# Kernel optimization log

Measured on AMD Instinct MI355X. Metric: run time of the kernel, lower is better.

## Reference

```python
import jax, jax.numpy as jnp
import numpy as np

NA, NC = 5, 20          # num_anchors, num_classes
EPS, SLOPE = 1e-5, 0.1  # BatchNorm eps, LeakyReLU slope


def _conv(x, w, pad):
    return jax.lax.conv_general_dilated(
        x, w, (1, 1), [(pad, pad), (pad, pad)],
        dimension_numbers=("NCHW", "OIHW", "NCHW"))


def _cbl(x, w, g, b, m, v, pad):
    # Conv2dBatchLeaky: conv (no bias) + eval-mode BN + LeakyReLU(0.1)
    x = _conv(x, w, pad)
    scale = (g * jax.lax.rsqrt(v + EPS))[None, :, None, None]
    shift = (b - m * g * jax.lax.rsqrt(v + EPS))[None, :, None, None]
    x = x * scale + shift
    return jnp.where(x > 0, x, SLOPE * x)


def _reorg(x, s=2):
    # faithful lightnet Reorg: out channels = s*s*C, spatial halved
    B, C, H, W = x.shape
    x = x.reshape(B, C, H // s, s, W // s, s)
    x = x.transpose(0, 1, 2, 4, 3, 5)                 # B,C,H/s,W/s,s,s
    x = x.reshape(B, C, (H // s) * (W // s), s * s)
    x = x.transpose(0, 1, 3, 2)                        # B,C,s*s,HW/s^2
    x = x.reshape(B, C, s * s, H // s, W // s)
    x = x.transpose(0, 2, 1, 3, 4)                     # B,s*s,C,H/s,W/s
    return x.reshape(B, s * s * C, H // s, W // s)


def setup_inputs() -> dict:
    key = jax.random.key(0)
    ks = jax.random.split(key, 16)
    B = 16
    return {
        "feat0": jax.random.normal(ks[0], (B, 1024, 19, 19), jnp.float32),
        "feat1": jax.random.normal(ks[1], (B, 512, 38, 38), jnp.float32),
        "w1": jax.random.normal(ks[2], (64, 512, 1, 1), jnp.float32) * 0.05,
        "g1": jax.random.uniform(ks[3], (64,), jnp.float32, 0.5, 1.5),
        "b1": jax.random.normal(ks[4], (64,), jnp.float32) * 0.05,
        "m1": jax.random.normal(ks[5], (64,), jnp.float32) * 0.05,
        "v1": jax.random.uniform(ks[6], (64,), jnp.float32, 0.5, 1.5),
        "w2": jax.random.normal(ks[7], (1024, 1280, 3, 3), jnp.float32) * 0.01,
        "g2": jax.random.uniform(ks[8], (1024,), jnp.float32, 0.5, 1.5),
        "b2": jax.random.normal(ks[9], (1024,), jnp.float32) * 0.05,
        "m2": jax.random.normal(ks[10], (1024,), jnp.float32) * 0.05,
        "v2": jax.random.uniform(ks[11], (1024,), jnp.float32, 0.5, 1.5),
        "wd": jax.random.normal(ks[12], (30, 1024, 1, 1), jnp.float32) * 0.02,
        "bd": jax.random.normal(ks[13], (30,), jnp.float32) * 0.02,
    }


def reference(feat0, feat1, w1, g1, b1, m1, v1, w2, g2, b2, m2, v2, wd, bd):
    stage6_reorg = _reorg(_cbl(feat1, w1, g1, b1, m1, v1, pad=0))   # B,256,19,19
    pre = _cbl(jnp.concatenate([stage6_reorg, feat0], axis=1),
               w2, g2, b2, m2, v2, pad=1)                            # B,1024,19,19
    B, C, H, W = pre.shape
    # one-hot reweighting mask: channel c belongs to class (c mod NC)
    rew = (jnp.mod(jnp.arange(C, dtype=jnp.float32), NC)[None, :]
           == jnp.arange(NC, dtype=jnp.float32)[:, None]).astype(pre.dtype)  # NC,C
    tiled = pre[:, None] * rew[None, :, :, None, None]               # B,NC,C,H,W
    pred = _conv(tiled.reshape(B * NC, C, H, W), wd, pad=0) \
        + bd[None, :, None, None]                                    # B*NC,30,H,W
    gp = pred.reshape(B, NC, NA, 6, H, W).transpose(0, 2, 1, 3, 4, 5)  # B,NA,NC,6,H,W
    cls = gp[:, :, :, 5]                                             # B,NA,NC,H,W
    ids = jnp.argmax(cls, axis=2)                                    # B,NA,H,W
    g05 = jnp.take_along_axis(gp[:, :, :, :5],
                              ids[:, :, None, None], axis=2)[:, :, 0]  # B,NA,5,H,W
    final = jnp.concatenate([g05, cls], axis=2)                      # B,NA,25,H,W
    return final.reshape(B, NA * (5 + NC), H, W)
```

## Files before the change

kernel.cpp:

```cpp
#include <hip/hip_runtime.h>
#include <hip/hip_bf16.h>

#define EPSV 1e-5f
#define SLOPEV 0.1f
#define AS1 __attribute__((address_space(1)))
#define AS3 __attribute__((address_space(3)))

typedef __attribute__((ext_vector_type(8))) _Float16 h8;
typedef __attribute__((ext_vector_type(4))) float f32x4;
typedef unsigned int uint32;
typedef unsigned short ushort_t;

#define PLANE       ((size_t)18063360)
#define WSPLIT_OFF  ((size_t)36126720)
#define PRE_OFF     ((size_t)124968960)

#define APREC  28224
#define ABUF   56448
#define BOFF   112896
#define BBUF   24576
#define SMEMSZ 162048

__device__ __forceinline__ void split2_pack(const float* f, uint32* ph, uint32* pm) {
#pragma unroll
  for (int i = 0; i < 4; ++i) {
    float a = f[2 * i], b = f[2 * i + 1];
    _Float16 ha = (_Float16)a, hb = (_Float16)b;
    float ra = (a - (float)ha) * 2048.f;
    float rb = (b - (float)hb) * 2048.f;
    _Float16 ma = (_Float16)ra, mb = (_Float16)rb;
    ph[i] = (uint32)__builtin_bit_cast(ushort_t, ha) | ((uint32)__builtin_bit_cast(ushort_t, hb) << 16);
    pm[i] = (uint32)__builtin_bit_cast(ushort_t, ma) | ((uint32)__builtin_bit_cast(ushort_t, mb) << 16);
  }
}

__global__ __launch_bounds__(256) void k_conv1(
    const float* __restrict__ feat1, const float* __restrict__ w1,
    const float* __restrict__ g1, const float* __restrict__ b1,
    const float* __restrict__ m1, const float* __restrict__ v1,
    char* __restrict__ nbase)
{
  __shared__ __attribute__((aligned(16))) float S[16384];
  const int bid = blockIdx.x;
  const int bx = bid % 12, cqq = (bid / 12) & 1, b = bid / 24;
  const int t = threadIdx.x;

#pragma unroll
  for (int i = 0; i < 16; ++i) {
    int f4 = t + i * 256;
    int j = f4 >> 7, c4 = (f4 & 127) * 4;
    *(float4*)&S[j * 512 + c4] = *(const float4*)&w1[(cqq * 32 + j) * 512 + c4];
  }
  __syncthreads();

  const int cq16 = t >> 7;
  const int cq = cqq * 2 + cq16;
  const int p = bx * 128 + (t & 127);
  const int pp = p < 1444 ? p : 1443;
  const float* xp = feat1 + (size_t)(b * 512) * 1444 + pp;
  float acc[16];
#pragma unroll
  for (int j = 0; j < 16; ++j) acc[j] = 0.f;
#pragma unroll 2
  for (int c4 = 0; c4 < 512; c4 += 4) {
    float x0 = xp[(size_t)(c4 + 0) * 1444];
    float x1 = xp[(size_t)(c4 + 1) * 1444];
    float x2 = xp[(size_t)(c4 + 2) * 1444];
    float x3 = xp[(size_t)(c4 + 3) * 1444];
#pragma unroll
    for (int j = 0; j < 16; ++j) {
      float4 w = *(const float4*)&S[(cq16 * 16 + j) * 512 + c4];
      acc[j] = fmaf(x0, w.x, acc[j]);
      acc[j] = fmaf(x1, w.y, acc[j]);
      acc[j] = fmaf(x2, w.z, acc[j]);
      acc[j] = fmaf(x3, w.w, acc[j]);
    }
  }
  if (p >= 1444) return;
#pragma unroll
  for (int j = 0; j < 16; ++j) {
    int co = cq * 16 + j;
    float sc = g1[co] / sqrtf(v1[co] + EPSV);
    float sh = b1[co] - m1[co] * sc;
    float v = fmaf(acc[j], sc, sh);
    acc[j] = v > 0.f ? v : SLOPEV * v;
  }
  int y = p / 38, x = p - (p / 38) * 38;
  int q = ((y & 1) << 1) | (x & 1);
  int s = (1 + (y >> 1)) * 21 + 1 + (x >> 1);
  const int sw = (s >> 1) & 3;
  size_t rowb = ((size_t)(b * 441 + s)) * 2560;
  int grp = (q * 64 + cq * 16) >> 5;
  char* d0 = nbase + rowb + grp * 64;
#pragma unroll
  for (int u = 0; u < 2; ++u) {
    int q4 = ((cq & 1) << 1) | u;
    uint32 H[4], M[4];
    split2_pack(&acc[u * 8], H, M);
    int off = (q4 ^ sw) << 4;
    *(uint4*)(d0 + off)         = make_uint4(H[0], H[1], H[2], H[3]);
    *(uint4*)(d0 + PLANE + off) = make_uint4(M[0], M[1], M[2], M[3]);
  }
}

__global__ __launch_bounds__(256) void k_prep(
    const float* __restrict__ feat0, const float* __restrict__ w2,
    char* __restrict__ nbase, char* __restrict__ wsp)
{
  __shared__ __attribute__((aligned(16))) float S[8192];
  const int bid = blockIdx.x;
  const int t = threadIdx.x;

  if (bid < 1600) {
    int gid = bid * 256 + t;
    int c16 = gid % 160;
    int r = gid / 160;
    int bp = r % 80;
    int pi = r / 80;
    int s;
    if (bp < 21) s = bp;
    else if (bp < 42) s = 399 + bp;
    else if (bp < 61) s = (bp - 41) * 21;
    else s = (bp - 60) * 21 + 20;
    int plane = pi >> 4, img = pi & 15;
    *(uint4*)(nbase + (size_t)plane * PLANE + ((size_t)(img * 441 + s)) * 2560 + c16 * 16)
        = make_uint4(0u, 0u, 0u, 0u);

  } else if (bid < 4160) {
    const int blk = bid - 1600;
    const int cc = blk >> 6, nt = (blk >> 2) & 15, nj = blk & 3;
    const float* src = w2 + ((size_t)(nt * 64 + nj * 16) * 1280 + cc * 32) * 9;
#pragma unroll
    for (int i = 0; i < 18; ++i) {
      int idx = t + i * 256;
      int col = idx / 288, d = idx - col * 288;
      S[col * 289 + d] = src[(size_t)col * 11520 + d];
    }
    __syncthreads();
#pragma unroll
    for (int it = 0; it < 3; ++it) {
      int u = t + it * 256;
      if (u < 576) {
        int tap = u / 64, kq = (u >> 4) & 3, ln = u & 15;
        float f[8];
#pragma unroll
        for (int c8 = 0; c8 < 8; ++c8) f[c8] = S[ln * 289 + (kq * 8 + c8) * 9 + tap] * 32.f;
        uint32 H[4], M[4];
        split2_pack(f, H, M);
        size_t ob = ((size_t)(cc * 16 + nt) * 9 + tap) * 8192 + nj * 1024
                  + (kq * 16 + ln) * 16;
        *(uint4*)(wsp + ob)        = make_uint4(H[0], H[1], H[2], H[3]);
        *(uint4*)(wsp + ob + 4096) = make_uint4(M[0], M[1], M[2], M[3]);
      }
    }

  } else {
    const int bid4 = bid - 4160;
    const int px = bid4 % 6, cy = (bid4 / 6) % 16, b = bid4 / 96;
    const int p0 = px * 64, c0 = 256 + cy * 64;
#pragma unroll
    for (int j = 0; j < 16; ++j) {
      int c_l = (t >> 6) + j * 4;
      int p_l = t & 63;
      float v = 0.f;
      int pos = p0 + p_l;
      if (pos < 361)
        v = feat0[((size_t)(b * 1024 + (c0 - 256) + c_l)) * 361 + pos];
      S[c_l * 65 + p_l] = v;
    }
    __syncthreads();
#pragma unroll
    for (int jj = 0; jj < 2; ++jj) {
      int p_l = (t >> 3) + jj * 32;
      int cgrp = t & 7;
      int pos = p0 + p_l;
      if (pos < 361) {
        int y = pos / 19, x = pos - (pos / 19) * 19;
        int s = (y + 1) * 21 + x + 1;
        float f[8];
#pragma unroll
        for (int u = 0; u < 8; ++u) f[u] = S[(cgrp * 8 + u) * 65 + p_l];
        uint32 H[4], M[4];
        split2_pack(f, H, M);
        int ch8 = c0 + cgrp * 8;
        int grp = ch8 >> 5, q4 = (ch8 >> 3) & 3;
        size_t byteo = ((size_t)(b * 441 + s)) * 2560 + grp * 64
                     + ((q4 ^ ((s >> 1) & 3)) << 4);
        *(uint4*)(nbase + byteo)         = make_uint4(H[0], H[1], H[2], H[3]);
        *(uint4*)(nbase + PLANE + byteo) = make_uint4(M[0], M[1], M[2], M[3]);
      }
    }
  }
}

__global__ __launch_bounds__(512, 2) void k_conv2(
    const char* __restrict__ nbase, const char* __restrict__ wsp,
    const float* __restrict__ g2, const float* __restrict__ b2,
    const float* __restrict__ m2, const float* __restrict__ v2,
    float* __restrict__ pre)
{
  __shared__ __attribute__((aligned(16))) unsigned char smem[SMEMSZ];

  const int bid = blockIdx.x;
  const int img = (bid & 7) * 2 + ((bid >> 3) & 1);
  const int ntile = (bid >> 4) & 15;
  const int co0 = ntile * 64;

  const int tid = threadIdx.x;
  const int wv = tid >> 6;
  const int lane = tid & 63;
  const int ln = lane & 15;
  const int q = lane >> 4;

  int arow[3];
#pragma unroll
  for (int mi = 0; mi < 3; ++mi) {
    int p = wv * 48 + mi * 16 + ln;
    p = p > 360 ? 360 : p;
    arow[mi] = (p / 19) * 21 + (p - (p / 19) * 19);
  }

  f32x4 acc0[3][4], acc1[3][4];
#pragma unroll
  for (int mi = 0; mi < 3; ++mi)
#pragma unroll
    for (int nj = 0; nj < 4; ++nj) { acc0[mi][nj] = (f32x4)0.f; acc1[mi][nj] = (f32x4)0.f; }

  const size_t imgbase = (size_t)(img * 441) * 2560;
  const size_t wnt = (size_t)ntile * 9 * 8192;

#pragma unroll
  for (int i = 0; i < 7; ++i) {
    int idx = tid + i * 512;
    if (idx < 3528) {
      int pr = idx / 1764;
      int r  = idx - pr * 1764;
      const char* src = nbase + (size_t)pr * PLANE + imgbase
                      + (size_t)(r >> 2) * 2560 + ((r & 3) << 4);
      __builtin_amdgcn_global_load_lds((const AS1 uint32*)src,
          (AS3 uint32*)(smem + idx * 16), 16, 0, 0);
    }
  }
  {
    const char* bs = wsp + wnt;
#pragma unroll
    for (int i = 0; i < 3; ++i) {
      int idx = tid + i * 512;
      __builtin_amdgcn_global_load_lds((const AS1 uint32*)(bs + idx * 16),
          (AS3 uint32*)(smem + BOFF + idx * 16), 16, 0, 0);
    }
  }
  __syncthreads();

#pragma unroll 1
  for (int cc = 0; cc < 1280; cc += 32) {
    const int cur = (cc >> 5) & 1;
    const unsigned char* aCur = smem + cur * ABUF;
    char* aNext = (char*)smem + (cur ^ 1) * ABUF;
    const int ccn = cc + 32;
    const bool pn = ccn < 1280;

#pragma unroll
    for (int p = 0; p < 3; ++p) {
      const int P = (cc >> 5) * 3 + p;
      if (P + 1 < 120) {
        const int nc = (P + 1) / 3, ntb = ((P + 1) - nc * 3) * 3;
        const char* bs = wsp + ((size_t)nc * 144 + (size_t)ntb) * 8192 + wnt;
        char* bd = (char*)smem + BOFF + ((P + 1) & 1) * BBUF;
#pragma unroll
        for (int i = 0; i < 3; ++i) {
          int idx = tid + i * 512;
          __builtin_amdgcn_global_load_lds((const AS1 uint32*)(bs + idx * 16),
              (AS3 uint32*)(bd + idx * 16), 16, 0, 0);
        }
      }
      if (pn) {
#pragma unroll
        for (int i = 0; i < 3; ++i) {
          int idx = p * 1176 + i * 512 + tid;
          if (idx < (p + 1) * 1176) {
            int pr = idx / 1764;
            int r  = idx - pr * 1764;
            const char* src = nbase + (size_t)pr * PLANE + imgbase
                            + (size_t)(r >> 2) * 2560 + (ccn << 1) + ((r & 3) << 4);
            __builtin_amdgcn_global_load_lds((const AS1 uint32*)src,
                (AS3 uint32*)(aNext + idx * 16), 16, 0, 0);
          }
        }
      }

      const unsigned char* bufR = smem + BOFF + (P & 1) * BBUF;
      __builtin_amdgcn_s_setprio(1);
#pragma unroll
      for (int t3 = 0; t3 < 3; ++t3) {
        const int trow = p * 21 + t3;
        h8 A0[3], A1[3];
#pragma unroll
        for (int mi = 0; mi < 3; ++mi) {
          int srow = arow[mi] + trow;
          int aoff = srow * 64 + ((q ^ ((srow >> 1) & 3)) << 4);
          A0[mi] = *(const h8*)(aCur + aoff);
          A1[mi] = *(const h8*)(aCur + APREC + aoff);
        }
#pragma unroll
        for (int nj = 0; nj < 4; ++nj) {
          const unsigned char* bp0 = bufR + t3 * 8192 + nj * 1024 + lane * 16;
          h8 B0 = *(const h8*)(bp0);
          h8 B1 = *(const h8*)(bp0 + 4096);
#pragma unroll
          for (int mi = 0; mi < 3; ++mi) {
            acc0[mi][nj] = __builtin_amdgcn_mfma_f32_16x16x32_f16(A0[mi], B0, acc0[mi][nj], 0, 0, 0);
            acc1[mi][nj] = __builtin_amdgcn_mfma_f32_16x16x32_f16(A0[mi], B1, acc1[mi][nj], 0, 0, 0);
            acc1[mi][nj] = __builtin_amdgcn_mfma_f32_16x16x32_f16(A1[mi], B0, acc1[mi][nj], 0, 0, 0);
          }
        }
      }
      __builtin_amdgcn_s_setprio(0);
      __syncthreads();
    }
  }

#pragma unroll
  for (int nj = 0; nj < 4; ++nj) {
    int co = co0 + nj * 16 + ln;
    float sc = g2[co] / sqrtf(v2[co] + EPSV) * 0.03125f;
    float sh = b2[co] - m2[co] * (sc * 32.f);
    float* op = pre + ((size_t)(img * 1024 + co)) * 361;
#pragma unroll
    for (int mi = 0; mi < 3; ++mi) {
#pragma unroll
      for (int r = 0; r < 4; ++r) {
        int p = wv * 48 + mi * 16 + q * 4 + r;
        if (p < 361) {
          float t = fmaf(acc1[mi][nj][r], 4.8828125e-4f, acc0[mi][nj][r]);
          float v = fmaf(t, sc, sh);
          v = v > 0.f ? v : SLOPEV * v;
          op[p] = v;
        }
      }
    }
  }
}

__global__ __launch_bounds__(384) void k_pred(
    const float* __restrict__ pre, const float* __restrict__ wd,
    const float* __restrict__ bd, float* __restrict__ pred)
{
  __shared__ float W[30 * 52];
  const int k = blockIdx.x;
  const int b = blockIdx.y;
  const int t = threadIdx.x;
  const int nj = (1023 - k) / 20 + 1;

  for (int u = t; u < 30 * 52; u += 384) {
    int o = u / 52, j = u - o * 52;
    W[u] = (j < nj) ? wd[o * 1024 + k + 20 * j] : 0.f;
  }
  __syncthreads();
  if (t >= 361) return;

  const float* xb = pre + (size_t)b * 1024 * 361 + t;
  float acc[30];
#pragma unroll
  for (int o = 0; o < 30; ++o) acc[o] = 0.f;
  for (int j = 0; j < nj; ++j) {
    float x = xb[(size_t)(k + 20 * j) * 361];
#pragma unroll
    for (int o = 0; o < 30; ++o) acc[o] = fmaf(W[o * 52 + j], x, acc[o]);
  }
  float* ob = pred + ((size_t)(b * 20 + k) * 30) * 361 + t;
#pragma unroll
  for (int o = 0; o < 30; ++o) ob[(size_t)o * 361] = acc[o] + bd[o];
}

__global__ __launch_bounds__(64) void k_sel(
    const float* __restrict__ pred, float* __restrict__ out)
{
  const int ph = blockIdx.x, a = blockIdx.y, b = blockIdx.z;
  const int p = ph * 64 + threadIdx.x;
  const bool act = p < 361;
  const int pp = act ? p : 360;
  const float* pb = pred + (size_t)b * 20 * 30 * 361 + pp;

  float best = -3.4e38f; int bidx = 0;
  float cls[20];
#pragma unroll
  for (int kk = 0; kk < 20; ++kk) {
    float s = pb[(size_t)(kk * 30 + a * 6 + 5) * 361];
    cls[kk] = s;
    if (s > best) { best = s; bidx = kk; }
  }
  if (!act) return;
#pragma unroll
  for (int kk = 0; kk < 20; ++kk)
    out[((size_t)(b * 125 + a * 25 + 5 + kk)) * 361 + p] = cls[kk];
#pragma unroll
  for (int j = 0; j < 5; ++j)
    out[((size_t)(b * 125 + a * 25 + j)) * 361 + p]
        = pb[(size_t)(bidx * 30 + a * 6 + j) * 361];
}

extern "C" void kernel_launch(void* const* d_in, const int* in_sizes, int n_in,
                              void* d_out, int out_size, void* d_ws, size_t ws_size,
                              hipStream_t stream)
{
  const float* feat0 = (const float*)d_in[0];
  const float* feat1 = (const float*)d_in[1];
  const float* w1    = (const float*)d_in[2];
  const float* g1    = (const float*)d_in[3];
  const float* b1    = (const float*)d_in[4];
  const float* m1    = (const float*)d_in[5];
  const float* v1    = (const float*)d_in[6];
  const float* w2    = (const float*)d_in[7];
  const float* g2    = (const float*)d_in[8];
  const float* b2    = (const float*)d_in[9];
  const float* m2    = (const float*)d_in[10];
  const float* v2    = (const float*)d_in[11];
  const float* wd    = (const float*)d_in[12];
  const float* bd    = (const float*)d_in[13];
  float* out = (float*)d_out;

  char*  nbase = (char*)d_ws;
  char*  wsp   = (char*)d_ws + WSPLIT_OFF;
  float* pre   = (float*)((char*)d_ws + PRE_OFF);
  float* pred  = (float*)((char*)d_ws + WSPLIT_OFF);

  k_conv1<<<dim3(384), 256, 0, stream>>>(feat1, w1, g1, b1, m1, v1, nbase);
  k_prep<<<dim3(5696), 256, 0, stream>>>(feat0, w2, nbase, wsp);
  k_conv2<<<dim3(256), 512, 0, stream>>>(nbase, wsp, g2, b2, m2, v2, pre);
  k_pred<<<dim3(20, 16), 384, 0, stream>>>(pre, wd, bd, pred);
  k_sel<<<dim3(6, 5, 16), 64, 0, stream>>>(pred, out);
}
```

Measured before the change: 432.8 us.

## Fold conv1 into prep kernel with two pixels per thread

The separate 1x1 conv1 kernel becomes the first 192 blocks of the k_prep launch, which removes one kernel launch and lets conv1 run alongside the zero-fill and weight-split blocks. Each thread now computes two pixel positions (128 apart), so the shared-memory weight reads are reused across twice the work and half as many blocks are needed. The cost is more registers per thread (32 accumulators) and a larger static shared allocation (64KB) for all k_prep blocks, which can cut occupancy of the other prep branches.

```diff
diff --git a/kernel.cpp b/kernel.cpp
--- a/kernel.cpp
+++ b/kernel.cpp
@@ -34,57 +34,8 @@
   }
 }
 
-__global__ __launch_bounds__(256) void k_conv1(
-    const float* __restrict__ feat1, const float* __restrict__ w1,
-    const float* __restrict__ g1, const float* __restrict__ b1,
-    const float* __restrict__ m1, const float* __restrict__ v1,
-    char* __restrict__ nbase)
-{
-  __shared__ __attribute__((aligned(16))) float S[16384];
-  const int bid = blockIdx.x;
-  const int bx = bid % 12, cqq = (bid / 12) & 1, b = bid / 24;
-  const int t = threadIdx.x;
-
-#pragma unroll
-  for (int i = 0; i < 16; ++i) {
-    int f4 = t + i * 256;
-    int j = f4 >> 7, c4 = (f4 & 127) * 4;
-    *(float4*)&S[j * 512 + c4] = *(const float4*)&w1[(cqq * 32 + j) * 512 + c4];
-  }
-  __syncthreads();
-
-  const int cq16 = t >> 7;
-  const int cq = cqq * 2 + cq16;
-  const int p = bx * 128 + (t & 127);
-  const int pp = p < 1444 ? p : 1443;
-  const float* xp = feat1 + (size_t)(b * 512) * 1444 + pp;
-  float acc[16];
-#pragma unroll
-  for (int j = 0; j < 16; ++j) acc[j] = 0.f;
-#pragma unroll 2
-  for (int c4 = 0; c4 < 512; c4 += 4) {
-    float x0 = xp[(size_t)(c4 + 0) * 1444];
-    float x1 = xp[(size_t)(c4 + 1) * 1444];
-    float x2 = xp[(size_t)(c4 + 2) * 1444];
-    float x3 = xp[(size_t)(c4 + 3) * 1444];
-#pragma unroll
-    for (int j = 0; j < 16; ++j) {
-      float4 w = *(const float4*)&S[(cq16 * 16 + j) * 512 + c4];
-      acc[j] = fmaf(x0, w.x, acc[j]);
-      acc[j] = fmaf(x1, w.y, acc[j]);
-      acc[j] = fmaf(x2, w.z, acc[j]);
-      acc[j] = fmaf(x3, w.w, acc[j]);
-    }
-  }
-  if (p >= 1444) return;
-#pragma unroll
-  for (int j = 0; j < 16; ++j) {
-    int co = cq * 16 + j;
-    float sc = g1[co] / sqrtf(v1[co] + EPSV);
-    float sh = b1[co] - m1[co] * sc;
-    float v = fmaf(acc[j], sc, sh);
-    acc[j] = v > 0.f ? v : SLOPEV * v;
-  }
+__device__ __forceinline__ void conv1_store(char* __restrict__ nbase, const float* acc,
+                                            int b, int p, int cq) {
   int y = p / 38, x = p - (p / 38) * 38;
   int q = ((y & 1) << 1) | (x & 1);
   int s = (1 + (y >> 1)) * 21 + 1 + (x >> 1);
@@ -104,15 +55,74 @@
 }
 
 __global__ __launch_bounds__(256) void k_prep(
+    const float* __restrict__ feat1, const float* __restrict__ w1,
+    const float* __restrict__ g1, const float* __restrict__ b1,
+    const float* __restrict__ m1, const float* __restrict__ v1,
     const float* __restrict__ feat0, const float* __restrict__ w2,
     char* __restrict__ nbase, char* __restrict__ wsp)
 {
-  __shared__ __attribute__((aligned(16))) float S[8192];
+  __shared__ __attribute__((aligned(16))) float S[16384];
   const int bid = blockIdx.x;
   const int t = threadIdx.x;
 
-  if (bid < 1600) {
-    int gid = bid * 256 + t;
+  if (bid < 192) {
+    const int bx = bid % 6, cqq = (bid / 6) & 1, b = bid / 12;
+#pragma unroll
+    for (int i = 0; i < 16; ++i) {
+      int f4 = t + i * 256;
+      int j = f4 >> 7, c4 = (f4 & 127) * 4;
+      *(float4*)&S[j * 512 + c4] = *(const float4*)&w1[(cqq * 32 + j) * 512 + c4];
+    }
+    __syncthreads();
+    const int t2 = t & 127;
+    const int cq16 = t >> 7;
+    const int cq = cqq * 2 + cq16;
+    const int pA = bx * 256 + t2;
+    const int pB = pA + 128;
+    const int ppB = pB < 1444 ? pB : 1443;
+    const float* xpA = feat1 + (size_t)(b * 512) * 1444 + pA;
+    const float* xpB = feat1 + (size_t)(b * 512) * 1444 + ppB;
+    float accA[16], accB[16];
+#pragma unroll
+    for (int j = 0; j < 16; ++j) { accA[j] = 0.f; accB[j] = 0.f; }
+#pragma unroll 2
+    for (int c4 = 0; c4 < 512; c4 += 4) {
+      float a0 = xpA[(size_t)(c4 + 0) * 1444];
+      float a1 = xpA[(size_t)(c4 + 1) * 1444];
+      float a2 = xpA[(size_t)(c4 + 2) * 1444];
+      float a3 = xpA[(size_t)(c4 + 3) * 1444];
+      float e0 = xpB[(size_t)(c4 + 0) * 1444];
+      float e1 = xpB[(size_t)(c4 + 1) * 1444];
+      float e2 = xpB[(size_t)(c4 + 2) * 1444];
+      float e3 = xpB[(size_t)(c4 + 3) * 1444];
+#pragma unroll
+      for (int j = 0; j < 16; ++j) {
+        float4 w = *(const float4*)&S[(cq16 * 16 + j) * 512 + c4];
+        accA[j] = fmaf(a0, w.x, accA[j]);
+        accA[j] = fmaf(a1, w.y, accA[j]);
+        accA[j] = fmaf(a2, w.z, accA[j]);
+        accA[j] = fmaf(a3, w.w, accA[j]);
+        accB[j] = fmaf(e0, w.x, accB[j]);
+        accB[j] = fmaf(e1, w.y, accB[j]);
+        accB[j] = fmaf(e2, w.z, accB[j]);
+        accB[j] = fmaf(e3, w.w, accB[j]);
+      }
+    }
+#pragma unroll
+    for (int j = 0; j < 16; ++j) {
+      int co = cq * 16 + j;
+      float sc = g1[co] / sqrtf(v1[co] + EPSV);
+      float sh = b1[co] - m1[co] * sc;
+      float va = fmaf(accA[j], sc, sh);
+      accA[j] = va > 0.f ? va : SLOPEV * va;
+      float vb = fmaf(accB[j], sc, sh);
+      accB[j] = vb > 0.f ? vb : SLOPEV * vb;
+    }
+    conv1_store(nbase, accA, b, pA, cq);
+    if (pB < 1444) conv1_store(nbase, accB, b, pB, cq);
+
+  } else if (bid < 1792) {
+    int gid = (bid - 192) * 256 + t;
     int c16 = gid % 160;
     int r = gid / 160;
     int bp = r % 80;
@@ -126,8 +136,8 @@
     *(uint4*)(nbase + (size_t)plane * PLANE + ((size_t)(img * 441 + s)) * 2560 + c16 * 16)
         = make_uint4(0u, 0u, 0u, 0u);
 
-  } else if (bid < 4160) {
-    const int blk = bid - 1600;
+  } else if (bid < 4352) {
+    const int blk = bid - 1792;
     const int cc = blk >> 6, nt = (blk >> 2) & 15, nj = blk & 3;
     const float* src = w2 + ((size_t)(nt * 64 + nj * 16) * 1280 + cc * 32) * 9;
 #pragma unroll
@@ -155,7 +165,7 @@
     }
 
   } else {
-    const int bid4 = bid - 4160;
+    const int bid4 = bid - 4352;
     const int px = bid4 % 6, cy = (bid4 / 6) % 16, b = bid4 / 96;
     const int p0 = px * 64, c0 = 256 + cy * 64;
 #pragma unroll
@@ -425,8 +435,7 @@
   float* pre   = (float*)((char*)d_ws + PRE_OFF);
   float* pred  = (float*)((char*)d_ws + WSPLIT_OFF);
 
-  k_conv1<<<dim3(384), 256, 0, stream>>>(feat1, w1, g1, b1, m1, v1, nbase);
-  k_prep<<<dim3(5696), 256, 0, stream>>>(feat0, w2, nbase, wsp);
+  k_prep<<<dim3(5888), 256, 0, stream>>>(feat1, w1, g1, b1, m1, v1, feat0, w2, nbase, wsp);
   k_conv2<<<dim3(256), 512, 0, stream>>>(nbase, wsp, g2, b2, m2, v2, pre);
   k_pred<<<dim3(20, 16), 384, 0, stream>>>(pre, wd, bd, pred);
   k_sel<<<dim3(6, 5, 16), 64, 0, stream>>>(pred, out);
```

After: 407.3 us. 5.9% less time.
